# Performance work log

Hardware: AMD Instinct MI355X
Metric: run time of the kernel (lower is better)

Reference implementation:

```python
import jax, jax.numpy as jnp
import numpy as np

B, T, IN, H, OUT = 64, 512, 256, 512, 256


def setup_inputs() -> dict:
    key = jax.random.key(0)
    ks = jax.random.split(key, 12)
    s_in = 1.0 / np.sqrt(H)  # PyTorch RNN init scale (uniform +-1/sqrt(H))
    u = lambda k, shape: jax.random.uniform(k, shape, jnp.float32, -s_in, s_in)
    return {
        "x": jax.random.normal(ks[0], (B, T, IN), jnp.float32),
        "W_ih0": u(ks[1], (H, IN)),
        "W_hh0": u(ks[2], (H, H)),
        "b_ih0": u(ks[3], (H,)),
        "b_hh0": u(ks[4], (H,)),
        "W_ih1": u(ks[5], (H, H)),
        "W_hh1": u(ks[6], (H, H)),
        "b_ih1": u(ks[7], (H,)),
        "b_hh1": u(ks[8], (H,)),
        "W_out": u(ks[9], (OUT, H)),
        "b_out": u(ks[10], (OUT,)),
    }


def _rnn_layer(seq, W_ih, W_hh, b_ih, b_hh):
    # seq: [B, T, D_in] -> outputs [B, T, H], last hidden [B, H]
    # Precompute input projection for all steps (one big GEMM).
    xp = jnp.einsum('btd,hd->bth', seq, W_ih) + b_ih + b_hh  # [B, T, H]
    xp_t = jnp.swapaxes(xp, 0, 1)  # [T, B, H] for scan over time
    h0 = jnp.zeros((seq.shape[0], W_hh.shape[0]), seq.dtype)

    def step(h, xpt):
        h = jnp.tanh(xpt + h @ W_hh.T)
        return h, h

    h_last, hs = jax.lax.scan(step, h0, xp_t)
    return jnp.swapaxes(hs, 0, 1), h_last


def reference(x, W_ih0, W_hh0, b_ih0, b_hh0, W_ih1, W_hh1, b_ih1, b_hh1, W_out, b_out):
    out0, _ = _rnn_layer(x, W_ih0, W_hh0, b_ih0, b_hh0)
    _, h_last = _rnn_layer(out0, W_ih1, W_hh1, b_ih1, b_hh1)
    return h_last @ W_out.T + b_out  # [B, OUT]
```

## Files before the change

### kernel.cpp

```cpp
#include <hip/hip_runtime.h>
#include <cmath>

#define B_   64
#define T_   512
#define IN_  256
#define H_   512
#define OUT_ 256
#define M_   (B_*T_)

typedef __bf16 bf16x4 __attribute__((ext_vector_type(4)));
typedef __bf16 bf16x8 __attribute__((ext_vector_type(8)));
typedef float  f32x4  __attribute__((ext_vector_type(4)));

static __device__ __forceinline__ void split_f32(float x, __bf16 &hi, __bf16 &lo) {
    unsigned u  = __float_as_uint(x);
    unsigned hu = u & 0xffff0000u;
    hi = __builtin_bit_cast(__bf16, (unsigned short)(hu >> 16));
    lo = (__bf16)(x - __uint_as_float(hu));
}

__global__ void split_arr(const float* __restrict__ src, __bf16* __restrict__ hi,
                          __bf16* __restrict__ lo, int n) {
    int i = blockIdx.x * 256 + threadIdx.x;
    if (i < n) { __bf16 h, l; split_f32(src[i], h, l); hi[i] = h; lo[i] = l; }
}

__global__ void bias_comb(const float* __restrict__ a, const float* __restrict__ b,
                          float* __restrict__ o, int n) {
    int i = blockIdx.x * 256 + threadIdx.x;
    if (i < n) o[i] = a[i] + b[i];
}

#define GBM 128
#define GBN 64
#define GBK 32
#define LDA 40

__global__ __launch_bounds__(256) void gemm_xp(
    const float* __restrict__ A, const __bf16* __restrict__ Whi,
    const __bf16* __restrict__ Wlo, const float* __restrict__ bias,
    float* __restrict__ C, int K)
{
    __shared__ __bf16 sAhi[GBM*LDA], sAlo[GBM*LDA], sBhi[GBN*LDA], sBlo[GBN*LDA];
    const int tid = threadIdx.x;
    const int m0 = blockIdx.y * GBM, n0 = blockIdx.x * GBN;
    const int wave = tid >> 6, lane = tid & 63, lm = lane & 15, q = lane >> 4;

    f32x4 acc[2][4];
#pragma unroll
    for (int i = 0; i < 2; ++i)
#pragma unroll
        for (int j = 0; j < 4; ++j) acc[i][j] = (f32x4){0.f,0.f,0.f,0.f};

    for (int k0 = 0; k0 < K; k0 += GBK) {
        __syncthreads();
#pragma unroll
        for (int i = 0; i < 4; ++i) {
            int c = tid + i * 256;
            int row = c >> 3, pos = c & 7;
            float4 v = *(const float4*)(&A[(size_t)(m0+row)*K + k0 + pos*4]);
            __bf16 h0,l0,h1,l1,h2,l2,h3,l3;
            split_f32(v.x,h0,l0); split_f32(v.y,h1,l1);
            split_f32(v.z,h2,l2); split_f32(v.w,h3,l3);
            *(bf16x4*)(&sAhi[row*LDA + pos*4]) = (bf16x4){h0,h1,h2,h3};
            *(bf16x4*)(&sAlo[row*LDA + pos*4]) = (bf16x4){l0,l1,l2,l3};
        }
        {
            int row = tid >> 2, pos = (tid & 3) * 8;
            *(bf16x8*)(&sBhi[row*LDA + pos]) =
                *(const bf16x8*)(&Whi[(size_t)(n0+row)*K + k0 + pos]);
            *(bf16x8*)(&sBlo[row*LDA + pos]) =
                *(const bf16x8*)(&Wlo[(size_t)(n0+row)*K + k0 + pos]);
        }
        __syncthreads();

        bf16x8 ah[2], al[2], bh[4], bl[4];
#pragma unroll
        for (int mt = 0; mt < 2; ++mt) {
            int r = wave*32 + mt*16 + lm;
            ah[mt] = *(const bf16x8*)(&sAhi[r*LDA + q*8]);
            al[mt] = *(const bf16x8*)(&sAlo[r*LDA + q*8]);
        }
#pragma unroll
        for (int nt = 0; nt < 4; ++nt) {
            int r = nt*16 + lm;
            bh[nt] = *(const bf16x8*)(&sBhi[r*LDA + q*8]);
            bl[nt] = *(const bf16x8*)(&sBlo[r*LDA + q*8]);
        }
#pragma unroll
        for (int mt = 0; mt < 2; ++mt)
#pragma unroll
            for (int nt = 0; nt < 4; ++nt) {
                acc[mt][nt] = __builtin_amdgcn_mfma_f32_16x16x32_bf16(ah[mt], bh[nt], acc[mt][nt], 0,0,0);
                acc[mt][nt] = __builtin_amdgcn_mfma_f32_16x16x32_bf16(ah[mt], bl[nt], acc[mt][nt], 0,0,0);
                acc[mt][nt] = __builtin_amdgcn_mfma_f32_16x16x32_bf16(al[mt], bh[nt], acc[mt][nt], 0,0,0);
            }
    }
#pragma unroll
    for (int mt = 0; mt < 2; ++mt)
#pragma unroll
        for (int nt = 0; nt < 4; ++nt)
#pragma unroll
            for (int r = 0; r < 4; ++r) {
                int m = m0 + wave*32 + mt*16 + q*4 + r;
                int n = n0 + nt*16 + lm;
                C[(size_t)m*H_ + n] = acc[mt][nt][r] + bias[n];
            }
}

#define RLDA 520

__global__ __launch_bounds__(256, 1) void rnn_fused(
    float* __restrict__ xp,
    const __bf16* __restrict__ w0hi, const __bf16* __restrict__ w0lo,
    const __bf16* __restrict__ wphi, const __bf16* __restrict__ wplo,
    const __bf16* __restrict__ w1hi, const __bf16* __restrict__ w1lo,
    const float* __restrict__ bias1,
    unsigned* __restrict__ hr0,
    unsigned* __restrict__ h1pk,
    float* __restrict__ hlast,
    int* __restrict__ flags)
{
    __shared__ __bf16 sAhi[16*RLDA], sAlo[16*RLDA];
    const int tid  = threadIdx.x;
    const int role = blockIdx.x >> 5;
    const int sub  = blockIdx.x & 31;
    const int g    = sub >> 3;
    const int c    = sub & 7;
    const int m0g  = g * 16;
    const int n0   = c * 64;
    const int wave = tid >> 6, lane = tid & 63, lm = lane & 15, q = lane >> 4;
    const int ncol = n0 + wave*16 + lm;
    const int srow = tid >> 4, sseg = tid & 15;

    int* const flag0 = flags + (0*4 + g)*16;
    int* const flagP = flags + (1*4 + g)*16;
    int* const flag1 = flags + (2*4 + g)*16;

    const __bf16* Wh = (role == 0) ? w0hi : (role == 1) ? wphi : w1hi;
    const __bf16* Wl = (role == 0) ? w0lo : (role == 1) ? wplo : w1lo;
    bf16x8 wh[16], wl[16];
#pragma unroll
    for (int kt = 0; kt < 16; ++kt) {
        wh[kt] = *(const bf16x8*)(&Wh[(size_t)ncol*H_ + kt*32 + q*8]);
        wl[kt] = *(const bf16x8*)(&Wl[(size_t)ncol*H_ + kt*32 + q*8]);
    }

    unsigned* const xpu = (unsigned*)xp;

    auto stage_slice = [&](const unsigned* hbase) {
        const unsigned long long* src =
            (const unsigned long long*)(hbase + (size_t)(m0g + srow)*H_);
        unsigned long long vv[16];
#pragma unroll
        for (int j = 0; j < 16; ++j)
            vv[j] = __hip_atomic_load(&src[sseg + j*16], __ATOMIC_RELAXED,
                                      __HIP_MEMORY_SCOPE_AGENT);
        __bf16* dh = &sAhi[srow*RLDA];
        __bf16* dl = &sAlo[srow*RLDA];
#pragma unroll
        for (int j = 0; j < 16; ++j) {
            unsigned p0 = (unsigned)vv[j], p1 = (unsigned)(vv[j] >> 32);
            *(unsigned*)(dh + (sseg + j*16)*2) = (p0 >> 16) | (p1 & 0xffff0000u);
            *(unsigned*)(dl + (sseg + j*16)*2) = (p0 & 0xffffu) | (p1 << 16);
        }
    };
    auto mma_tile = [&]() {
        f32x4 acc = (f32x4){0.f,0.f,0.f,0.f};
#pragma unroll
        for (int kt = 0; kt < 16; ++kt) {
            bf16x8 ah = *(const bf16x8*)(&sAhi[lm*RLDA + kt*32 + q*8]);
            bf16x8 al = *(const bf16x8*)(&sAlo[lm*RLDA + kt*32 + q*8]);
            acc = __builtin_amdgcn_mfma_f32_16x16x32_bf16(ah, wh[kt], acc, 0,0,0);
            acc = __builtin_amdgcn_mfma_f32_16x16x32_bf16(ah, wl[kt], acc, 0,0,0);
            acc = __builtin_amdgcn_mfma_f32_16x16x32_bf16(al, wh[kt], acc, 0,0,0);
        }
        return acc;
    };
    auto publish = [&](unsigned* dst, int m, float hv) {
        __bf16 hh, hl; split_f32(hv, hh, hl);
        unsigned pk = ((unsigned)__builtin_bit_cast(unsigned short, hh) << 16)
                    |  (unsigned)__builtin_bit_cast(unsigned short, hl);
        __hip_atomic_store(&dst[(size_t)m*H_ + ncol], pk,
                           __ATOMIC_RELAXED, __HIP_MEMORY_SCOPE_AGENT);
    };

    if (role == 0) {
        for (int t = 0; t < T_; ++t) {
            float xr[4];
#pragma unroll
            for (int r = 0; r < 4; ++r)
                xr[r] = xp[((size_t)(m0g + q*4 + r)*T_ + t)*H_ + ncol];
            if (t && tid == 0) {
                for (;;) {
                    bool ok = true;
#pragma unroll
                    for (int i = 0; i < 8; ++i)
                        ok &= (__hip_atomic_load(&flag0[i], __ATOMIC_RELAXED,
                                                 __HIP_MEMORY_SCOPE_AGENT) >= t);
                    if (ok) break;
                    __builtin_amdgcn_s_sleep(1);
                }
            }
            __syncthreads();
            stage_slice(hr0 + (size_t)t*(B_*H_));
            __syncthreads();
            f32x4 acc = mma_tile();
            unsigned* dst = hr0 + (size_t)(t+1)*(B_*H_);
#pragma unroll
            for (int r = 0; r < 4; ++r) {
                int m = m0g + q*4 + r;
                float hv = tanhf(xr[r] + acc[r]);
                publish(dst, m, hv);
            }
            __syncthreads();
            if (tid == 0)
                __hip_atomic_store(&flag0[c], t+1, __ATOMIC_RELEASE,
                                   __HIP_MEMORY_SCOPE_AGENT);
        }
    } else if (role == 1) {
        const float b1 = bias1[ncol];
        for (int t = 0; t < T_; ++t) {
            if (tid == 0) {
                for (;;) {
                    bool ok = true;
#pragma unroll
                    for (int i = 0; i < 8; ++i)
                        ok &= (__hip_atomic_load(&flag0[i], __ATOMIC_RELAXED,
                                                 __HIP_MEMORY_SCOPE_AGENT) >= t+1);
                    if (ok) break;
                    __builtin_amdgcn_s_sleep(1);
                }
            }
            __syncthreads();
            stage_slice(hr0 + (size_t)(t+1)*(B_*H_));
            __syncthreads();
            f32x4 acc = mma_tile();
#pragma unroll
            for (int r = 0; r < 4; ++r) {
                int m = m0g + q*4 + r;
                float v = acc[r] + b1;
                __hip_atomic_store(&xpu[((size_t)m*T_ + t)*H_ + ncol],
                                   __float_as_uint(v),
                                   __ATOMIC_RELAXED, __HIP_MEMORY_SCOPE_AGENT);
            }
            __syncthreads();
            if (tid == 0)
                __hip_atomic_store(&flagP[c], t+1, __ATOMIC_RELEASE,
                                   __HIP_MEMORY_SCOPE_AGENT);
        }
    } else {
        for (int t = 0; t < T_; ++t) {
            if (tid == 0) {
                for (;;) {
                    bool ok = true;
#pragma unroll
                    for (int i = 0; i < 8; ++i)
                        ok &= (__hip_atomic_load(&flagP[i], __ATOMIC_RELAXED,
                                                 __HIP_MEMORY_SCOPE_AGENT) >= t+1);
                    if (t)
#pragma unroll
                        for (int i = 0; i < 8; ++i)
                            ok &= (__hip_atomic_load(&flag1[i], __ATOMIC_RELAXED,
                                                     __HIP_MEMORY_SCOPE_AGENT) >= t);
                    if (ok) break;
                    __builtin_amdgcn_s_sleep(1);
                }
            }
            __syncthreads();
            float xr[4];
#pragma unroll
            for (int r = 0; r < 4; ++r)
                xr[r] = __uint_as_float(__hip_atomic_load(
                    &xpu[((size_t)(m0g + q*4 + r)*T_ + t)*H_ + ncol],
                    __ATOMIC_RELAXED, __HIP_MEMORY_SCOPE_AGENT));
            stage_slice(h1pk + (size_t)(t & 1)*(B_*H_));
            __syncthreads();
            f32x4 acc = mma_tile();
            unsigned* dst = h1pk + (size_t)((t+1) & 1)*(B_*H_);
#pragma unroll
            for (int r = 0; r < 4; ++r) {
                int m = m0g + q*4 + r;
                float hv = tanhf(xr[r] + acc[r]);
                publish(dst, m, hv);
                if (t == T_-1) hlast[(size_t)m*H_ + ncol] = hv;
            }
            __syncthreads();
            if (tid == 0)
                __hip_atomic_store(&flag1[c], t+1, __ATOMIC_RELEASE,
                                   __HIP_MEMORY_SCOPE_AGENT);
        }
    }
}

__global__ __launch_bounds__(256) void out_proj(
    const float* __restrict__ hlast, const float* __restrict__ Wout,
    const float* __restrict__ bout, float* __restrict__ out)
{
    __shared__ float sh[H_];
    int b = blockIdx.x;
    for (int i = threadIdx.x; i < H_; i += 256) sh[i] = hlast[(size_t)b*H_ + i];
    __syncthreads();
    int o = threadIdx.x;
    const float* wr = &Wout[(size_t)o*H_];
    float acc = 0.f;
#pragma unroll 4
    for (int k = 0; k < H_; k += 4) {
        float4 wv = *(const float4*)(&wr[k]);
        acc += wv.x*sh[k] + wv.y*sh[k+1] + wv.z*sh[k+2] + wv.w*sh[k+3];
    }
    out[(size_t)b*OUT_ + o] = bout[o] + acc;
}

extern "C" void kernel_launch(void* const* d_in, const int* in_sizes, int n_in,
                              void* d_out, int out_size, void* d_ws, size_t ws_size,
                              hipStream_t stream)
{
    const float* x    = (const float*)d_in[0];
    const float* Wih0 = (const float*)d_in[1];
    const float* Whh0 = (const float*)d_in[2];
    const float* bih0 = (const float*)d_in[3];
    const float* bhh0 = (const float*)d_in[4];
    const float* Wih1 = (const float*)d_in[5];
    const float* Whh1 = (const float*)d_in[6];
    const float* bih1 = (const float*)d_in[7];
    const float* bhh1 = (const float*)d_in[8];
    const float* Wout = (const float*)d_in[9];
    const float* bout = (const float*)d_in[10];

    char* w = (char*)d_ws;
    size_t off = 0;
    auto alloc = [&](size_t bytes) -> void* {
        void* p = w + off; off = (off + bytes + 255) & ~(size_t)255; return p;
    };
    float*    xp    = (float*)   alloc((size_t)M_*H_*4);
    unsigned* hr0   = (unsigned*)alloc((size_t)(T_+1)*B_*H_*4);
    __bf16* wih0hi = (__bf16*)alloc((size_t)H_*IN_*2);
    __bf16* wih0lo = (__bf16*)alloc((size_t)H_*IN_*2);
    __bf16* whh0hi = (__bf16*)alloc((size_t)H_*H_*2);
    __bf16* whh0lo = (__bf16*)alloc((size_t)H_*H_*2);
    __bf16* wih1hi = (__bf16*)alloc((size_t)H_*H_*2);
    __bf16* wih1lo = (__bf16*)alloc((size_t)H_*H_*2);
    __bf16* whh1hi = (__bf16*)alloc((size_t)H_*H_*2);
    __bf16* whh1lo = (__bf16*)alloc((size_t)H_*H_*2);
    float*  bias0  = (float*) alloc(H_*4);
    float*  bias1  = (float*) alloc(H_*4);
    size_t zstart = off;
    unsigned* h1pk = (unsigned*)alloc((size_t)2*B_*H_*4);
    int*    flags  = (int*)   alloc(768);
    size_t zlen = off - zstart;
    float*  hlast  = (float*) alloc((size_t)B_*H_*4);

    hipMemsetAsync(w + zstart, 0, zlen, stream);
    hipMemsetAsync(hr0, 0, (size_t)B_*H_*4, stream);

    split_arr<<<(H_*IN_+255)/256, 256, 0, stream>>>(Wih0, wih0hi, wih0lo, H_*IN_);
    split_arr<<<(H_*H_ +255)/256, 256, 0, stream>>>(Whh0, whh0hi, whh0lo, H_*H_);
    split_arr<<<(H_*H_ +255)/256, 256, 0, stream>>>(Wih1, wih1hi, wih1lo, H_*H_);
    split_arr<<<(H_*H_ +255)/256, 256, 0, stream>>>(Whh1, whh1hi, whh1lo, H_*H_);
    bias_comb<<<2, 256, 0, stream>>>(bih0, bhh0, bias0, H_);
    bias_comb<<<2, 256, 0, stream>>>(bih1, bhh1, bias1, H_);

    dim3 ggrid(H_/GBN, M_/GBM);
    gemm_xp<<<ggrid, 256, 0, stream>>>(x, wih0hi, wih0lo, bias0, xp, IN_);

    rnn_fused<<<96, 256, 0, stream>>>(xp, whh0hi, whh0lo, wih1hi, wih1lo,
                                      whh1hi, whh1lo, bias1, hr0, h1pk, hlast, flags);

    out_proj<<<B_, 256, 0, stream>>>(hlast, Wout, bout, (float*)d_out);
}
```

Baseline: 2.761 ms.

## Replace flag barriers with sequence-tagged data polling over ring buffers

Each published hidden-state and projection value now carries its timestep as a 32-bit tag in a 64-bit word. Consumers poll the data itself instead of waiting on per-step flag counters, which removes a round trip of flag store, flag poll and barrier from the per-step critical path. Full-history and xp-sized buffers become 8-deep rings, with coarse back-pressure flags that allow producers to run ahead by up to the ring depth. In exchange, every transfer is twice as wide, and correctness depends on relaxed 64-bit atomics being observed as whole words and on the ring depth preventing overwrites.

```diff
diff --git a/kernel.cpp b/kernel.cpp
--- a/kernel.cpp
+++ b/kernel.cpp
@@ -11,6 +11,7 @@
 typedef __bf16 bf16x4 __attribute__((ext_vector_type(4)));
 typedef __bf16 bf16x8 __attribute__((ext_vector_type(8)));
 typedef float  f32x4  __attribute__((ext_vector_type(4)));
+typedef unsigned long long u64;
 
 static __device__ __forceinline__ void split_f32(float x, __bf16 &hi, __bf16 &lo) {
     unsigned u  = __float_as_uint(x);
@@ -109,15 +110,17 @@
 }
 
 #define RLDA 520
+#define RDEP 8
 
 __global__ __launch_bounds__(256, 1) void rnn_fused(
-    float* __restrict__ xp,
+    const float* __restrict__ xp0,
     const __bf16* __restrict__ w0hi, const __bf16* __restrict__ w0lo,
     const __bf16* __restrict__ wphi, const __bf16* __restrict__ wplo,
     const __bf16* __restrict__ w1hi, const __bf16* __restrict__ w1lo,
     const float* __restrict__ bias1,
-    unsigned* __restrict__ hr0,
-    unsigned* __restrict__ h1pk,
+    u64* __restrict__ h0ring,
+    u64* __restrict__ xp1ring,
+    u64* __restrict__ h1ring,
     float* __restrict__ hlast,
     int* __restrict__ flags)
 {
@@ -133,9 +136,8 @@
     const int ncol = n0 + wave*16 + lm;
     const int srow = tid >> 4, sseg = tid & 15;
 
-    int* const flag0 = flags + (0*4 + g)*16;
-    int* const flagP = flags + (1*4 + g)*16;
-    int* const flag1 = flags + (2*4 + g)*16;
+    int* const flagP = flags + g*16;
+    int* const flag1 = flags + 64 + g*16;
 
     const __bf16* Wh = (role == 0) ? w0hi : (role == 1) ? wphi : w1hi;
     const __bf16* Wl = (role == 0) ? w0lo : (role == 1) ? wplo : w1lo;
@@ -146,23 +148,25 @@
         wl[kt] = *(const bf16x8*)(&Wl[(size_t)ncol*H_ + kt*32 + q*8]);
     }
 
-    unsigned* const xpu = (unsigned*)xp;
-
-    auto stage_slice = [&](const unsigned* hbase) {
-        const unsigned long long* src =
-            (const unsigned long long*)(hbase + (size_t)(m0g + srow)*H_);
-        unsigned long long vv[16];
-#pragma unroll
-        for (int j = 0; j < 16; ++j)
-            vv[j] = __hip_atomic_load(&src[sseg + j*16], __ATOMIC_RELAXED,
-                                      __HIP_MEMORY_SCOPE_AGENT);
-        __bf16* dh = &sAhi[srow*RLDA];
-        __bf16* dl = &sAlo[srow*RLDA];
-#pragma unroll
-        for (int j = 0; j < 16; ++j) {
-            unsigned p0 = (unsigned)vv[j], p1 = (unsigned)(vv[j] >> 32);
-            *(unsigned*)(dh + (sseg + j*16)*2) = (p0 >> 16) | (p1 & 0xffff0000u);
-            *(unsigned*)(dl + (sseg + j*16)*2) = (p0 & 0xffffu) | (p1 << 16);
+    auto stage_poll = [&](const u64* slot, unsigned target) {
+        const u64* row = slot + (size_t)(m0g + srow) * H_;
+        __bf16* dh = &sAhi[srow * RLDA];
+        __bf16* dl = &sAlo[srow * RLDA];
+        unsigned pend = 0xffffu;
+        while (pend) {
+#pragma unroll
+            for (int j = 0; j < 16; ++j)
+                if (pend & (1u << j)) {
+                    int c0 = (sseg + j*16) * 2;
+                    u64 a = __hip_atomic_load(&row[c0],   __ATOMIC_RELAXED, __HIP_MEMORY_SCOPE_AGENT);
+                    u64 b = __hip_atomic_load(&row[c0+1], __ATOMIC_RELAXED, __HIP_MEMORY_SCOPE_AGENT);
+                    if ((unsigned)(a >> 32) == target && (unsigned)(b >> 32) == target) {
+                        unsigned pa = (unsigned)a, pb = (unsigned)b;
+                        *(unsigned*)(dh + c0) = (pa >> 16) | (pb & 0xffff0000u);
+                        *(unsigned*)(dl + c0) = (pa & 0xffffu) | (pb << 16);
+                        pend &= ~(1u << j);
+                    }
+                }
         }
     };
     auto mma_tile = [&]() {
@@ -177,12 +181,11 @@
         }
         return acc;
     };
-    auto publish = [&](unsigned* dst, int m, float hv) {
+    auto pack_h = [&](float hv, unsigned seq) -> u64 {
         __bf16 hh, hl; split_f32(hv, hh, hl);
         unsigned pk = ((unsigned)__builtin_bit_cast(unsigned short, hh) << 16)
                     |  (unsigned)__builtin_bit_cast(unsigned short, hl);
-        __hip_atomic_store(&dst[(size_t)m*H_ + ncol], pk,
-                           __ATOMIC_RELAXED, __HIP_MEMORY_SCOPE_AGENT);
+        return ((u64)seq << 32) | pk;
     };
 
     if (role == 0) {
@@ -190,105 +193,121 @@
             float xr[4];
 #pragma unroll
             for (int r = 0; r < 4; ++r)
-                xr[r] = xp[((size_t)(m0g + q*4 + r)*T_ + t)*H_ + ncol];
-            if (t && tid == 0) {
-                for (;;) {
-                    bool ok = true;
+                xr[r] = xp0[((size_t)(m0g + q*4 + r)*T_ + t)*H_ + ncol];
+            const int tgt = t - (RDEP - 1);
+            int f[8];
+            if (tid == 0 && tgt > 0)
+#pragma unroll
+                for (int i = 0; i < 8; ++i)
+                    f[i] = __hip_atomic_load(&flagP[i], __ATOMIC_RELAXED, __HIP_MEMORY_SCOPE_AGENT);
+
+            stage_poll(h0ring + (size_t)(t & 7)*(B_*H_), (unsigned)t);
+            __syncthreads();
+            f32x4 acc = mma_tile();
+            u64 pv[4];
+#pragma unroll
+            for (int r = 0; r < 4; ++r)
+                pv[r] = pack_h(tanhf(xr[r] + acc[r]), (unsigned)(t+1));
+
+            if (tid == 0 && tgt > 0) {
+                bool ok = true;
+#pragma unroll
+                for (int i = 0; i < 8; ++i) ok &= (f[i] >= tgt);
+                while (!ok) {
+                    __builtin_amdgcn_s_sleep(1);
+                    ok = true;
 #pragma unroll
                     for (int i = 0; i < 8; ++i)
-                        ok &= (__hip_atomic_load(&flag0[i], __ATOMIC_RELAXED,
-                                                 __HIP_MEMORY_SCOPE_AGENT) >= t);
-                    if (ok) break;
-                    __builtin_amdgcn_s_sleep(1);
+                        ok &= (__hip_atomic_load(&flagP[i], __ATOMIC_RELAXED,
+                                                 __HIP_MEMORY_SCOPE_AGENT) >= tgt);
                 }
             }
             __syncthreads();
-            stage_slice(hr0 + (size_t)t*(B_*H_));
-            __syncthreads();
-            f32x4 acc = mma_tile();
-            unsigned* dst = hr0 + (size_t)(t+1)*(B_*H_);
-#pragma unroll
-            for (int r = 0; r < 4; ++r) {
-                int m = m0g + q*4 + r;
-                float hv = tanhf(xr[r] + acc[r]);
-                publish(dst, m, hv);
-            }
-            __syncthreads();
-            if (tid == 0)
-                __hip_atomic_store(&flag0[c], t+1, __ATOMIC_RELEASE,
-                                   __HIP_MEMORY_SCOPE_AGENT);
+
+            u64* dst = h0ring + (size_t)((t+1) & 7)*(B_*H_);
+#pragma unroll
+            for (int r = 0; r < 4; ++r)
+                __hip_atomic_store(&dst[(size_t)(m0g + q*4 + r)*H_ + ncol], pv[r],
+                                   __ATOMIC_RELAXED, __HIP_MEMORY_SCOPE_AGENT);
         }
     } else if (role == 1) {
         const float b1 = bias1[ncol];
         for (int t = 0; t < T_; ++t) {
-            if (tid == 0) {
-                for (;;) {
-                    bool ok = true;
+            const int tgt = t - (RDEP - 1);
+            int f[8];
+            if (tid == 0 && tgt > 0)
+#pragma unroll
+                for (int i = 0; i < 8; ++i)
+                    f[i] = __hip_atomic_load(&flag1[i], __ATOMIC_RELAXED, __HIP_MEMORY_SCOPE_AGENT);
+
+            stage_poll(h0ring + (size_t)((t+1) & 7)*(B_*H_), (unsigned)(t+1));
+            __syncthreads();
+            f32x4 acc = mma_tile();
+            u64 pv[4];
+#pragma unroll
+            for (int r = 0; r < 4; ++r)
+                pv[r] = ((u64)(unsigned)(t+1) << 32) | __float_as_uint(acc[r] + b1);
+
+            if (tid == 0 && tgt > 0) {
+                bool ok = true;
+#pragma unroll
+                for (int i = 0; i < 8; ++i) ok &= (f[i] >= tgt);
+                while (!ok) {
+                    __builtin_amdgcn_s_sleep(1);
+                    ok = true;
 #pragma unroll
                     for (int i = 0; i < 8; ++i)
-                        ok &= (__hip_atomic_load(&flag0[i], __ATOMIC_RELAXED,
-                                                 __HIP_MEMORY_SCOPE_AGENT) >= t+1);
-                    if (ok) break;
-                    __builtin_amdgcn_s_sleep(1);
+                        ok &= (__hip_atomic_load(&flag1[i], __ATOMIC_RELAXED,
+                                                 __HIP_MEMORY_SCOPE_AGENT) >= tgt);
                 }
             }
             __syncthreads();
-            stage_slice(hr0 + (size_t)(t+1)*(B_*H_));
+
+            u64* dst = xp1ring + (size_t)(t & 7)*(B_*H_);
+#pragma unroll
+            for (int r = 0; r < 4; ++r)
+                __hip_atomic_store(&dst[(size_t)(m0g + q*4 + r)*H_ + ncol], pv[r],
+                                   __ATOMIC_RELAXED, __HIP_MEMORY_SCOPE_AGENT);
+            if (tid == 0)
+                __hip_atomic_store(&flagP[c], t+1, __ATOMIC_RELEASE, __HIP_MEMORY_SCOPE_AGENT);
+        }
+    } else {
+        for (int t = 0; t < T_; ++t) {
+            stage_poll(h1ring + (size_t)(t & 1)*(B_*H_), (unsigned)t);
+            u64 xv[4];
+            {
+                const u64* xs = xp1ring + (size_t)(t & 7)*(B_*H_);
+                unsigned pend = 0xfu;
+                while (pend) {
+#pragma unroll
+                    for (int r = 0; r < 4; ++r)
+                        if (pend & (1u << r)) {
+                            u64 v = __hip_atomic_load(&xs[(size_t)(m0g + q*4 + r)*H_ + ncol],
+                                                      __ATOMIC_RELAXED, __HIP_MEMORY_SCOPE_AGENT);
+                            if ((unsigned)(v >> 32) == (unsigned)(t+1)) { xv[r] = v; pend &= ~(1u << r); }
+                        }
+                }
+            }
             __syncthreads();
             f32x4 acc = mma_tile();
+            float hv[4]; u64 pv[4];
+#pragma unroll
+            for (int r = 0; r < 4; ++r) {
+                hv[r] = tanhf(__uint_as_float((unsigned)xv[r]) + acc[r]);
+                pv[r] = pack_h(hv[r], (unsigned)(t+1));
+            }
+            __syncthreads();
+
+            u64* dst = h1ring + (size_t)((t+1) & 1)*(B_*H_);
 #pragma unroll
             for (int r = 0; r < 4; ++r) {
                 int m = m0g + q*4 + r;
-                float v = acc[r] + b1;
-                __hip_atomic_store(&xpu[((size_t)m*T_ + t)*H_ + ncol],
-                                   __float_as_uint(v),
+                __hip_atomic_store(&dst[(size_t)m*H_ + ncol], pv[r],
                                    __ATOMIC_RELAXED, __HIP_MEMORY_SCOPE_AGENT);
-            }
-            __syncthreads();
+                if (t == T_-1) hlast[(size_t)m*H_ + ncol] = hv[r];
+            }
             if (tid == 0)
-                __hip_atomic_store(&flagP[c], t+1, __ATOMIC_RELEASE,
-                                   __HIP_MEMORY_SCOPE_AGENT);
-        }
-    } else {
-        for (int t = 0; t < T_; ++t) {
-            if (tid == 0) {
-                for (;;) {
-                    bool ok = true;
-#pragma unroll
-                    for (int i = 0; i < 8; ++i)
-                        ok &= (__hip_atomic_load(&flagP[i], __ATOMIC_RELAXED,
-                                                 __HIP_MEMORY_SCOPE_AGENT) >= t+1);
-                    if (t)
-#pragma unroll
-                        for (int i = 0; i < 8; ++i)
-                            ok &= (__hip_atomic_load(&flag1[i], __ATOMIC_RELAXED,
-                                                     __HIP_MEMORY_SCOPE_AGENT) >= t);
-                    if (ok) break;
-                    __builtin_amdgcn_s_sleep(1);
-                }
-            }
-            __syncthreads();
-            float xr[4];
-#pragma unroll
-            for (int r = 0; r < 4; ++r)
-                xr[r] = __uint_as_float(__hip_atomic_load(
-                    &xpu[((size_t)(m0g + q*4 + r)*T_ + t)*H_ + ncol],
-                    __ATOMIC_RELAXED, __HIP_MEMORY_SCOPE_AGENT));
-            stage_slice(h1pk + (size_t)(t & 1)*(B_*H_));
-            __syncthreads();
-            f32x4 acc = mma_tile();
-            unsigned* dst = h1pk + (size_t)((t+1) & 1)*(B_*H_);
-#pragma unroll
-            for (int r = 0; r < 4; ++r) {
-                int m = m0g + q*4 + r;
-                float hv = tanhf(xr[r] + acc[r]);
-                publish(dst, m, hv);
-                if (t == T_-1) hlast[(size_t)m*H_ + ncol] = hv;
-            }
-            __syncthreads();
-            if (tid == 0)
-                __hip_atomic_store(&flag1[c], t+1, __ATOMIC_RELEASE,
-                                   __HIP_MEMORY_SCOPE_AGENT);
+                __hip_atomic_store(&flag1[c], t+1, __ATOMIC_RELEASE, __HIP_MEMORY_SCOPE_AGENT);
         }
     }
 }
@@ -333,8 +352,7 @@
     auto alloc = [&](size_t bytes) -> void* {
         void* p = w + off; off = (off + bytes + 255) & ~(size_t)255; return p;
     };
-    float*    xp    = (float*)   alloc((size_t)M_*H_*4);
-    unsigned* hr0   = (unsigned*)alloc((size_t)(T_+1)*B_*H_*4);
+    float*  xp     = (float*) alloc((size_t)M_*H_*4);
     __bf16* wih0hi = (__bf16*)alloc((size_t)H_*IN_*2);
     __bf16* wih0lo = (__bf16*)alloc((size_t)H_*IN_*2);
     __bf16* whh0hi = (__bf16*)alloc((size_t)H_*H_*2);
@@ -346,13 +364,14 @@
     float*  bias0  = (float*) alloc(H_*4);
     float*  bias1  = (float*) alloc(H_*4);
     size_t zstart = off;
-    unsigned* h1pk = (unsigned*)alloc((size_t)2*B_*H_*4);
-    int*    flags  = (int*)   alloc(768);
+    u64*    h0ring = (u64*)   alloc((size_t)RDEP*B_*H_*8);
+    u64*    xp1ring= (u64*)   alloc((size_t)RDEP*B_*H_*8);
+    u64*    h1ring = (u64*)   alloc((size_t)2*B_*H_*8);
+    int*    flags  = (int*)   alloc(512);
     size_t zlen = off - zstart;
     float*  hlast  = (float*) alloc((size_t)B_*H_*4);
 
     hipMemsetAsync(w + zstart, 0, zlen, stream);
-    hipMemsetAsync(hr0, 0, (size_t)B_*H_*4, stream);
 
     split_arr<<<(H_*IN_+255)/256, 256, 0, stream>>>(Wih0, wih0hi, wih0lo, H_*IN_);
     split_arr<<<(H_*H_ +255)/256, 256, 0, stream>>>(Whh0, whh0hi, whh0lo, H_*H_);
@@ -365,7 +384,8 @@
     gemm_xp<<<ggrid, 256, 0, stream>>>(x, wih0hi, wih0lo, bias0, xp, IN_);
 
     rnn_fused<<<96, 256, 0, stream>>>(xp, whh0hi, whh0lo, wih1hi, wih1lo,
-                                      whh1hi, whh1lo, bias1, hr0, h1pk, hlast, flags);
+                                      whh1hi, whh1lo, bias1,
+                                      h0ring, xp1ring, h1ring, hlast, flags);
 
     out_proj<<<B_, 256, 0, stream>>>(hlast, Wout, bout, (float*)d_out);
 }
```

After: 4.909 ms. +77.8%, slower.
